# Performance work log

Measured on AMD Instinct MI355X. Metric: run time of the kernel, lower is better.

The kernel has to match this reference:

```python
import jax, jax.numpy as jnp
import numpy as np
import math

DIM = 512
B, T, H, W = 1, 8, 64, 64


def setup_inputs() -> dict:
    key = jax.random.key(0)
    k0, k1, k2 = jax.random.split(key, 3)
    x = jax.random.normal(k0, (B, DIM, T, H, W), dtype=jnp.float32)
    gamma = jnp.ones((DIM,), jnp.float32)                      # RMS_norm gamma (viewed as flat vector)
    w_qkv = jax.random.normal(k1, (3 * DIM, DIM), jnp.float32) * 0.02  # conv1x1 weight (out, in)
    b_qkv = jnp.zeros((3 * DIM,), jnp.float32)
    w_proj = jax.random.normal(k2, (DIM, DIM), jnp.float32) * 0.02     # zero-init in torch; random for a meaningful baseline
    b_proj = jnp.zeros((DIM,), jnp.float32)
    return dict(x=x, gamma=gamma, w_qkv=w_qkv, b_qkv=b_qkv, w_proj=w_proj, b_proj=b_proj)


def reference(x, gamma, w_qkv, b_qkv, w_proj, b_proj):
    b, c, t, h, w = x.shape
    xt = jnp.transpose(x, (0, 2, 3, 4, 1))          # [b, t, h, w, c]
    identity = xt
    y = xt.reshape(b * t, h, w, c)
    # RMS_norm: L2 norm over channels (last dim), clamped, scaled by sqrt(c)*gamma
    norm = jnp.clip(jnp.linalg.norm(y, axis=-1, keepdims=True), 1e-12, None)
    y = y / norm * (c ** 0.5) * gamma
    # 1x1 conv QKV as GEMM over channels
    qkv = jnp.einsum('bhwc,oc->bhwo', y, w_qkv) + b_qkv        # [bt, h, w, 3c]
    qkv = qkv.reshape(b * t, h * w, 1, 3 * c)                  # nh=1 per source rearrange
    q, k, v = jnp.split(qkv, 3, axis=-1)                       # each [bt, hw, 1, c]
    scale = 1.0 / math.sqrt(c)
    # NOTE: hw sits in the batch position (faithful to source); seq len = nh = 1
    attn = jnp.einsum('bsnc,bsmc->bsnm', q, k) * scale         # [bt, hw, 1, 1]
    attn = jax.nn.softmax(attn, axis=-1)                       # trivially 1.0
    o = jnp.einsum('bsnm,bsmc->bsnc', attn, v)                 # == v
    o = o.reshape(b * t, h, w, c)
    o = jnp.einsum('bhwc,oc->bhwo', o, w_proj) + b_proj        # 1x1 proj conv
    o = o.reshape(b, t, h, w, c)
    out = jnp.transpose(o + identity, (0, 4, 1, 2, 3))         # back to [b, c, t, h, w]
    return out
```

## Files before the change

kernel.cpp:

```cpp
#include <hip/hip_runtime.h>

typedef unsigned short ushort_t;
typedef __attribute__((ext_vector_type(8))) short short8;
typedef __attribute__((ext_vector_type(4))) float f32x4;

#define DIMC 512
#define PN   32768
#define SQRTC 22.627416997969522f

__device__ __forceinline__ ushort_t f2bf(float f) {
  unsigned int u = __float_as_uint(f);
  unsigned int r = u + 0x7fffu + ((u >> 16) & 1u);
  return (ushort_t)(r >> 16);
}

__device__ __forceinline__ int kkey(int r) { return (r & 7) ^ ((r >> 2) & 7); }

__device__ __forceinline__ uint4 pack8(float4 a, float4 b) {
  union { ushort_t u[8]; uint4 v; } r;
  r.u[0] = f2bf(a.x); r.u[1] = f2bf(a.y); r.u[2] = f2bf(a.z); r.u[3] = f2bf(a.w);
  r.u[4] = f2bf(b.x); r.u[5] = f2bf(b.y); r.u[6] = f2bf(b.z); r.u[7] = f2bf(b.w);
  return r.v;
}

__global__ __launch_bounds__(256) void k_wgemm(
    const float* __restrict__ wproj,
    const float* __restrict__ wqkv,
    const float* __restrict__ bqkv,
    const float* __restrict__ bproj,
    const float* __restrict__ gamma,
    ushort_t* __restrict__ Mp2,
    float* __restrict__ fb) {
  int bid = blockIdx.x, tid = threadIdx.x;
  if (bid >= 16) {
    int wave = tid >> 6, lane = tid & 63;
    int o = (bid - 16) * 4 + wave;
    float part = 0.f;
#pragma unroll
    for (int i = 0; i < 8; ++i) {
      int k = lane + i * 64;
      part += wproj[o * DIMC + k] * bqkv[1024 + k];
    }
    for (int off = 32; off; off >>= 1) part += __shfl_down(part, off, 64);
    if (lane == 0) fb[o] = part + bproj[o];
    return;
  }

  __shared__ ushort_t As[128 * 64];
  __shared__ ushort_t Bs[128 * 64];
  int c0 = (bid & 3) * 128;
  int o0 = (bid >> 2) * 128;
  int wave = tid >> 6, lane = tid & 63;
  int wo = (wave & 1) * 64, wp = (wave >> 1) * 64;
  int q = lane >> 4, ln = lane & 15;

  f32x4 zero = {0.f, 0.f, 0.f, 0.f};
  f32x4 acc[4][4];
#pragma unroll
  for (int i = 0; i < 4; ++i)
#pragma unroll
    for (int j = 0; j < 4; ++j) acc[i][j] = zero;

  int sr = tid >> 3;
  int sc = tid & 7;
  const float* Ag = wproj + (long)(o0 + sr) * DIMC + sc * 8;
  int kr = tid >> 5;
  int c4 = (tid & 31) * 4;

  for (int kc = 0; kc < DIMC; kc += 64) {
    __syncthreads();
#pragma unroll
    for (int it = 0; it < 4; ++it) {
      int r = sr + it * 32;
      float4 a0 = *(const float4*)(Ag + (long)it * 32 * DIMC + kc);
      float4 a1 = *(const float4*)(Ag + (long)it * 32 * DIMC + kc + 4);
      *(uint4*)(&As[r * 64 + ((sc ^ (r & 7)) * 8)]) = pack8(a0, a1);
    }
#pragma unroll
    for (int ps = 0; ps < 8; ++ps) {
      int k = kc + ps * 8 + kr;
      float4 b = *(const float4*)(wqkv + (long)(1024 + k) * DIMC + c0 + c4);
      char* bsb = (char*)Bs;
      ushort_t e[4] = {f2bf(b.x), f2bf(b.y), f2bf(b.z), f2bf(b.w)};
#pragma unroll
      for (int i = 0; i < 4; ++i) {
        int c = c4 + i;
        *(ushort_t*)(bsb + c * 128 + ((ps ^ kkey(c)) * 16) + kr * 2) = e[i];
      }
    }
    __syncthreads();
#pragma unroll
    for (int ks = 0; ks < 2; ++ks) {
      int cch = ks * 4 + q;
      short8 af[4], bf[4];
#pragma unroll
      for (int mi = 0; mi < 4; ++mi) {
        int row = wo + mi * 16 + ln;
        af[mi] = *(const short8*)(&As[row * 64 + ((cch ^ (row & 7)) * 8)]);
      }
#pragma unroll
      for (int ni = 0; ni < 4; ++ni) {
        int row = wp + ni * 16 + ln;
        bf[ni] = *(const short8*)(&Bs[row * 64 + ((cch ^ kkey(row)) * 8)]);
      }
#pragma unroll
      for (int mi = 0; mi < 4; ++mi)
#pragma unroll
        for (int ni = 0; ni < 4; ++ni)
          acc[mi][ni] = __builtin_amdgcn_mfma_f32_16x16x32_bf16(af[mi], bf[ni], acc[mi][ni], 0, 0, 0);
    }
  }

#pragma unroll
  for (int mi = 0; mi < 4; ++mi) {
    int obase = o0 + wo + mi * 16 + q * 4;
#pragma unroll
    for (int ni = 0; ni < 4; ++ni) {
      int c = c0 + wp + ni * 16 + ln;
      float g = gamma[c];
      int kb2 = c >> 6, ks2 = (c >> 5) & 1, q2 = (c >> 3) & 3, j2 = c & 7;
#pragma unroll
      for (int r = 0; r < 4; ++r) {
        int o = obase + r;
        int w2 = o >> 6, mi2 = (o >> 4) & 3, ln2 = o & 15;
        long idx = (((((long)w2 * 8 + kb2) * 2 + ks2) * 4 + mi2) * 64 + q2 * 16 + ln2) * 8 + j2;
        Mp2[idx] = f2bf(acc[mi][ni][r] * g);
      }
    }
  }
}

__global__ __launch_bounds__(512, 2) void k_fused(
    const float* __restrict__ x,
    const ushort_t* __restrict__ Mp2,
    const float* __restrict__ fb,
    float* __restrict__ out) {
  __shared__ __align__(16) char smem[80256];
  ushort_t* xs = (ushort_t*)smem;
  float* ot    = (float*)smem;
  float* red   = (float*)(smem + 69632);
  float* s_sh  = (float*)(smem + 77952);
  float* fb_sh = (float*)(smem + 78208);
  int tid = threadIdx.x;
  long p0 = (long)blockIdx.x * 64;

  int wave = tid >> 6, lane = tid & 63;
  int q = lane >> 4, ln = lane & 15;
  int pl4 = (tid & 15) * 4;
  int kq  = tid >> 4;

  const ushort_t* Aw = Mp2 + (long)wave * 32768 + lane * 8;

  fb_sh[tid] = fb[tid];

  float4 v[16];
#pragma unroll
  for (int sw = 0; sw < 4; ++sw) {
    const float* xp = x + (long)(kq * 4 + sw * 128) * PN + p0 + pl4;
#pragma unroll
    for (int j = 0; j < 4; ++j)
      v[sw * 4 + j] = *(const float4*)(xp + (long)j * PN);
  }

  short8 afb[2][8];
#pragma unroll
  for (int f = 0; f < 8; ++f) afb[0][f] = *(const short8*)(Aw + f * 512);

  float ss0 = 0.f, ss1 = 0.f, ss2 = 0.f, ss3 = 0.f;
#pragma unroll
  for (int sw = 0; sw < 4; ++sw) {
    int k4 = kq * 4 + sw * 128;
    float4 v0 = v[sw * 4 + 0], v1 = v[sw * 4 + 1];
    float4 v2 = v[sw * 4 + 2], v3 = v[sw * 4 + 3];
    ss0 += v0.x * v0.x + v1.x * v1.x + v2.x * v2.x + v3.x * v3.x;
    ss1 += v0.y * v0.y + v1.y * v1.y + v2.y * v2.y + v3.y * v3.y;
    ss2 += v0.z * v0.z + v1.z * v1.z + v2.z * v2.z + v3.z * v3.z;
    ss3 += v0.w * v0.w + v1.w * v1.w + v2.w * v2.w + v3.w * v3.w;
    ushort_t t0[4] = {f2bf(v0.x), f2bf(v1.x), f2bf(v2.x), f2bf(v3.x)};
    ushort_t t1[4] = {f2bf(v0.y), f2bf(v1.y), f2bf(v2.y), f2bf(v3.y)};
    ushort_t t2[4] = {f2bf(v0.z), f2bf(v1.z), f2bf(v2.z), f2bf(v3.z)};
    ushort_t t3[4] = {f2bf(v0.w), f2bf(v1.w), f2bf(v2.w), f2bf(v3.w)};
    char* base = (char*)xs + (k4 >> 6) * 8192;
    int ch  = (k4 >> 3) & 7;
    int sub = (k4 & 7) * 2;
    *(uint2*)(base + (pl4 + 0) * 128 + ((ch ^ kkey(pl4 + 0)) * 16) + sub) = *(const uint2*)t0;
    *(uint2*)(base + (pl4 + 1) * 128 + ((ch ^ kkey(pl4 + 1)) * 16) + sub) = *(const uint2*)t1;
    *(uint2*)(base + (pl4 + 2) * 128 + ((ch ^ kkey(pl4 + 2)) * 16) + sub) = *(const uint2*)t2;
    *(uint2*)(base + (pl4 + 3) * 128 + ((ch ^ kkey(pl4 + 3)) * 16) + sub) = *(const uint2*)t3;
  }
  red[kq * 65 + pl4 + 0] = ss0;
  red[kq * 65 + pl4 + 1] = ss1;
  red[kq * 65 + pl4 + 2] = ss2;
  red[kq * 65 + pl4 + 3] = ss3;
  __syncthreads();

  if (tid < 64) {
    float t = 0.f;
#pragma unroll
    for (int g = 0; g < 32; ++g) t += red[g * 65 + tid];
    s_sh[tid] = SQRTC / fmaxf(sqrtf(t), 1e-12f);
  }

  f32x4 zero = {0.f, 0.f, 0.f, 0.f};
  f32x4 acc[4][4];
#pragma unroll
  for (int i = 0; i < 4; ++i)
#pragma unroll
    for (int j = 0; j < 4; ++j) acc[i][j] = zero;

#pragma unroll
  for (int kb = 0; kb < 8; ++kb) {
    if (kb < 7) {
#pragma unroll
      for (int f = 0; f < 8; ++f)
        afb[(kb + 1) & 1][f] = *(const short8*)(Aw + ((kb + 1) * 8 + f) * 512);
    }
    const char* bbase = (const char*)xs + kb * 8192;
#pragma unroll
    for (int ks = 0; ks < 2; ++ks) {
      int cch = ks * 4 + q;
      short8 bfr[4];
#pragma unroll
      for (int ni = 0; ni < 4; ++ni) {
        int row = ni * 16 + ln;
        bfr[ni] = *(const short8*)(bbase + row * 128 + ((cch ^ kkey(row)) * 16));
      }
#pragma unroll
      for (int mi = 0; mi < 4; ++mi)
#pragma unroll
        for (int ni = 0; ni < 4; ++ni)
          acc[mi][ni] = __builtin_amdgcn_mfma_f32_16x16x32_bf16(
              afb[kb & 1][ks * 4 + mi], bfr[ni], acc[mi][ni], 0, 0, 0);
    }
  }
  __syncthreads();

  int ccmy = (kq >> 3) & 1;
  float s4x = s_sh[pl4 + 0], s4y = s_sh[pl4 + 1];
  float s4z = s_sh[pl4 + 2], s4w = s_sh[pl4 + 3];
#pragma unroll
  for (int cc = 0; cc < 2; ++cc) {
#pragma unroll
    for (int mm = 0; mm < 2; ++mm) {
      int mi = cc * 2 + mm;
      int rbase = wave * 32 + mm * 16 + q * 4;
#pragma unroll
      for (int ni = 0; ni < 4; ++ni)
#pragma unroll
        for (int r = 0; r < 4; ++r)
          ot[(rbase + r) * 68 + ni * 16 + ln] = acc[mi][ni][r];
    }
    __syncthreads();
    if (ccmy == cc) {
#pragma unroll
      for (int sw = 0; sw < 4; ++sw)
#pragma unroll
        for (int j = 0; j < 4; ++j) {
          int o = kq * 4 + sw * 128 + j;
          int r_loc = (o >> 6) * 32 + (o & 31);
          const float* gp = ot + r_loc * 68 + pl4;
          float fbv = fb_sh[o];
          float4 xv = v[sw * 4 + j];
          f32x4 res;
          res[0] = xv.x + fbv + s4x * gp[0];
          res[1] = xv.y + fbv + s4y * gp[1];
          res[2] = xv.z + fbv + s4z * gp[2];
          res[3] = xv.w + fbv + s4w * gp[3];
          __builtin_nontemporal_store(res, (f32x4*)(out + (long)o * PN + p0 + pl4));
        }
    }
    if (cc == 0) __syncthreads();
  }
}

extern "C" void kernel_launch(void* const* d_in, const int* in_sizes, int n_in,
                              void* d_out, int out_size, void* d_ws, size_t ws_size,
                              hipStream_t stream) {
  const float* x     = (const float*)d_in[0];
  const float* gamma = (const float*)d_in[1];
  const float* wqkv  = (const float*)d_in[2];
  const float* bqkv  = (const float*)d_in[3];
  const float* wproj = (const float*)d_in[4];
  const float* bproj = (const float*)d_in[5];

  char* ws = (char*)d_ws;
  ushort_t* Mp2 = (ushort_t*)(ws);
  float*    fb  = (float*)(ws + 524288);

  k_wgemm<<<dim3(144), dim3(256), 0, stream>>>(wproj, wqkv, bqkv, bproj, gamma, Mp2, fb);
  k_fused<<<dim3(512), dim3(512), 0, stream>>>(x, Mp2, fb, (float*)d_out);
}
```

Before: 154.5 us.

## Split x load and bf16 staging into halves overlapped with GEMM k-blocks

The x tile load, sum-of-squares and bf16 LDS staging now run in two halves over channels. The first half is staged, then the second half's global loads are issued while the GEMM runs over the first four k-blocks, after which the second half is processed and the remaining k-blocks run. This aims to hide global-memory latency behind MFMA work instead of loading all 16 float4 values up front. It adds an extra barrier and changes instruction scheduling and register pressure.

```diff
diff --git a/kernel.cpp b/kernel.cpp
--- a/kernel.cpp
+++ b/kernel.cpp
@@ -154,40 +154,89 @@
   fb_sh[tid] = fb[tid];
 
   float4 v[16];
-#pragma unroll
-  for (int sw = 0; sw < 4; ++sw) {
-    const float* xp = x + (long)(kq * 4 + sw * 128) * PN + p0 + pl4;
-#pragma unroll
-    for (int j = 0; j < 4; ++j)
-      v[sw * 4 + j] = *(const float4*)(xp + (long)j * PN);
-  }
-
+  float ss0 = 0.f, ss1 = 0.f, ss2 = 0.f, ss3 = 0.f;
+  f32x4 zero = {0.f, 0.f, 0.f, 0.f};
+  f32x4 acc[4][4];
   short8 afb[2][8];
+
+#define LOADH(S0)                                                        \
+  {                                                                      \
+    _Pragma("unroll")                                                    \
+    for (int sw = (S0); sw < (S0) + 2; ++sw) {                           \
+      const float* xp = x + (long)(kq * 4 + sw * 128) * PN + p0 + pl4;   \
+      _Pragma("unroll")                                                  \
+      for (int j = 0; j < 4; ++j)                                        \
+        v[sw * 4 + j] = *(const float4*)(xp + (long)j * PN);             \
+    }                                                                    \
+  }
+
+#define PROCH(S0)                                                                      \
+  {                                                                                    \
+    _Pragma("unroll")                                                                  \
+    for (int sw = (S0); sw < (S0) + 2; ++sw) {                                         \
+      int k4 = kq * 4 + sw * 128;                                                      \
+      float4 v0 = v[sw * 4 + 0], v1 = v[sw * 4 + 1];                                   \
+      float4 v2 = v[sw * 4 + 2], v3 = v[sw * 4 + 3];                                   \
+      ss0 += v0.x * v0.x + v1.x * v1.x + v2.x * v2.x + v3.x * v3.x;                    \
+      ss1 += v0.y * v0.y + v1.y * v1.y + v2.y * v2.y + v3.y * v3.y;                    \
+      ss2 += v0.z * v0.z + v1.z * v1.z + v2.z * v2.z + v3.z * v3.z;                    \
+      ss3 += v0.w * v0.w + v1.w * v1.w + v2.w * v2.w + v3.w * v3.w;                    \
+      ushort_t t0[4] = {f2bf(v0.x), f2bf(v1.x), f2bf(v2.x), f2bf(v3.x)};               \
+      ushort_t t1[4] = {f2bf(v0.y), f2bf(v1.y), f2bf(v2.y), f2bf(v3.y)};               \
+      ushort_t t2[4] = {f2bf(v0.z), f2bf(v1.z), f2bf(v2.z), f2bf(v3.z)};               \
+      ushort_t t3[4] = {f2bf(v0.w), f2bf(v1.w), f2bf(v2.w), f2bf(v3.w)};               \
+      char* base = (char*)xs + (k4 >> 6) * 8192;                                       \
+      int ch  = (k4 >> 3) & 7;                                                         \
+      int sub = (k4 & 7) * 2;                                                          \
+      *(uint2*)(base + (pl4 + 0) * 128 + ((ch ^ kkey(pl4 + 0)) * 16) + sub) = *(const uint2*)t0; \
+      *(uint2*)(base + (pl4 + 1) * 128 + ((ch ^ kkey(pl4 + 1)) * 16) + sub) = *(const uint2*)t1; \
+      *(uint2*)(base + (pl4 + 2) * 128 + ((ch ^ kkey(pl4 + 2)) * 16) + sub) = *(const uint2*)t2; \
+      *(uint2*)(base + (pl4 + 3) * 128 + ((ch ^ kkey(pl4 + 3)) * 16) + sub) = *(const uint2*)t3; \
+    }                                                                                  \
+  }
+
+#define GEMMR(KB0, KB1)                                                          \
+  {                                                                              \
+    _Pragma("unroll")                                                            \
+    for (int kb = (KB0); kb < (KB1); ++kb) {                                     \
+      if (kb < 7) {                                                              \
+        _Pragma("unroll")                                                        \
+        for (int f = 0; f < 8; ++f)                                              \
+          afb[(kb + 1) & 1][f] = *(const short8*)(Aw + ((kb + 1) * 8 + f) * 512); \
+      }                                                                          \
+      const char* bbase = (const char*)xs + kb * 8192;                           \
+      _Pragma("unroll")                                                          \
+      for (int ks = 0; ks < 2; ++ks) {                                           \
+        int cch = ks * 4 + q;                                                    \
+        short8 bfr[4];                                                           \
+        _Pragma("unroll")                                                        \
+        for (int ni = 0; ni < 4; ++ni) {                                         \
+          int row = ni * 16 + ln;                                                \
+          bfr[ni] = *(const short8*)(bbase + row * 128 + ((cch ^ kkey(row)) * 16)); \
+        }                                                                        \
+        _Pragma("unroll")                                                        \
+        for (int mi = 0; mi < 4; ++mi)                                           \
+          _Pragma("unroll")                                                      \
+          for (int ni = 0; ni < 4; ++ni)                                         \
+            acc[mi][ni] = __builtin_amdgcn_mfma_f32_16x16x32_bf16(               \
+                afb[kb & 1][ks * 4 + mi], bfr[ni], acc[mi][ni], 0, 0, 0);        \
+      }                                                                          \
+    }                                                                            \
+  }
+
+  LOADH(0);
 #pragma unroll
   for (int f = 0; f < 8; ++f) afb[0][f] = *(const short8*)(Aw + f * 512);
-
-  float ss0 = 0.f, ss1 = 0.f, ss2 = 0.f, ss3 = 0.f;
-#pragma unroll
-  for (int sw = 0; sw < 4; ++sw) {
-    int k4 = kq * 4 + sw * 128;
-    float4 v0 = v[sw * 4 + 0], v1 = v[sw * 4 + 1];
-    float4 v2 = v[sw * 4 + 2], v3 = v[sw * 4 + 3];
-    ss0 += v0.x * v0.x + v1.x * v1.x + v2.x * v2.x + v3.x * v3.x;
-    ss1 += v0.y * v0.y + v1.y * v1.y + v2.y * v2.y + v3.y * v3.y;
-    ss2 += v0.z * v0.z + v1.z * v1.z + v2.z * v2.z + v3.z * v3.z;
-    ss3 += v0.w * v0.w + v1.w * v1.w + v2.w * v2.w + v3.w * v3.w;
-    ushort_t t0[4] = {f2bf(v0.x), f2bf(v1.x), f2bf(v2.x), f2bf(v3.x)};
-    ushort_t t1[4] = {f2bf(v0.y), f2bf(v1.y), f2bf(v2.y), f2bf(v3.y)};
-    ushort_t t2[4] = {f2bf(v0.z), f2bf(v1.z), f2bf(v2.z), f2bf(v3.z)};
-    ushort_t t3[4] = {f2bf(v0.w), f2bf(v1.w), f2bf(v2.w), f2bf(v3.w)};
-    char* base = (char*)xs + (k4 >> 6) * 8192;
-    int ch  = (k4 >> 3) & 7;
-    int sub = (k4 & 7) * 2;
-    *(uint2*)(base + (pl4 + 0) * 128 + ((ch ^ kkey(pl4 + 0)) * 16) + sub) = *(const uint2*)t0;
-    *(uint2*)(base + (pl4 + 1) * 128 + ((ch ^ kkey(pl4 + 1)) * 16) + sub) = *(const uint2*)t1;
-    *(uint2*)(base + (pl4 + 2) * 128 + ((ch ^ kkey(pl4 + 2)) * 16) + sub) = *(const uint2*)t2;
-    *(uint2*)(base + (pl4 + 3) * 128 + ((ch ^ kkey(pl4 + 3)) * 16) + sub) = *(const uint2*)t3;
-  }
+  PROCH(0);
+  __syncthreads();
+
+  LOADH(2);
+#pragma unroll
+  for (int i = 0; i < 4; ++i)
+#pragma unroll
+    for (int j = 0; j < 4; ++j) acc[i][j] = zero;
+  GEMMR(0, 4);
+  PROCH(2);
   red[kq * 65 + pl4 + 0] = ss0;
   red[kq * 65 + pl4 + 1] = ss1;
   red[kq * 65 + pl4 + 2] = ss2;
@@ -200,39 +249,7 @@
     for (int g = 0; g < 32; ++g) t += red[g * 65 + tid];
     s_sh[tid] = SQRTC / fmaxf(sqrtf(t), 1e-12f);
   }
-
-  f32x4 zero = {0.f, 0.f, 0.f, 0.f};
-  f32x4 acc[4][4];
-#pragma unroll
-  for (int i = 0; i < 4; ++i)
-#pragma unroll
-    for (int j = 0; j < 4; ++j) acc[i][j] = zero;
-
-#pragma unroll
-  for (int kb = 0; kb < 8; ++kb) {
-    if (kb < 7) {
-#pragma unroll
-      for (int f = 0; f < 8; ++f)
-        afb[(kb + 1) & 1][f] = *(const short8*)(Aw + ((kb + 1) * 8 + f) * 512);
-    }
-    const char* bbase = (const char*)xs + kb * 8192;
-#pragma unroll
-    for (int ks = 0; ks < 2; ++ks) {
-      int cch = ks * 4 + q;
-      short8 bfr[4];
-#pragma unroll
-      for (int ni = 0; ni < 4; ++ni) {
-        int row = ni * 16 + ln;
-        bfr[ni] = *(const short8*)(bbase + row * 128 + ((cch ^ kkey(row)) * 16));
-      }
-#pragma unroll
-      for (int mi = 0; mi < 4; ++mi)
-#pragma unroll
-        for (int ni = 0; ni < 4; ++ni)
-          acc[mi][ni] = __builtin_amdgcn_mfma_f32_16x16x32_bf16(
-              afb[kb & 1][ks * 4 + mi], bfr[ni], acc[mi][ni], 0, 0, 0);
-    }
-  }
+  GEMMR(4, 8);
   __syncthreads();
 
   int ccmy = (kq >> 3) & 1;
@@ -271,6 +288,9 @@
     }
     if (cc == 0) __syncthreads();
   }
+#undef LOADH
+#undef PROCH
+#undef GEMMR
 }
 
 extern "C" void kernel_launch(void* const* d_in, const int* in_sizes, int n_in,
```

New measurement: 152.6 us. About the same (-1.2%).
